# Kernel tuning notes

Hardware: AMD Instinct MI355X
Metric: run time of the kernel (lower is better)

The kernel has to match this reference:

```python
import jax, jax.numpy as jnp
import numpy as np

NEG_SLOPE = 0.2
BN_EPS = 1e-5


def setup_inputs() -> dict:
    key = jax.random.key(0)
    ks = jax.random.split(key, 10)
    N, E, F_IN, F_HID, F_OUT = 100000, 1600000, 64, 64, 32
    x = jax.random.normal(ks[0], (N, F_IN), dtype=jnp.float32)
    edge_index = jax.random.randint(ks[1], (2, E), 0, N, dtype=jnp.int64)
    s = 1.0 / np.sqrt(F_IN)
    W = jax.random.uniform(ks[2], (F_HID, F_IN), jnp.float32, -s, s)      # GATConv lin weight
    att_src = jax.random.uniform(ks[3], (F_HID,), jnp.float32, -s, s)
    att_dst = jax.random.uniform(ks[4], (F_HID,), jnp.float32, -s, s)
    conv_b = jnp.zeros((F_HID,), jnp.float32)
    gamma = jnp.ones((F_HID,), jnp.float32)
    beta = jnp.zeros((F_HID,), jnp.float32)
    s2 = 1.0 / np.sqrt(F_HID)
    fc_W = jax.random.uniform(ks[5], (F_OUT, F_HID), jnp.float32, -s2, s2)
    fc_b = jax.random.uniform(ks[6], (F_OUT,), jnp.float32, -s2, s2)
    return {"x": x, "edge_index": edge_index, "W": W, "att_src": att_src,
            "att_dst": att_dst, "conv_b": conv_b, "gamma": gamma, "beta": beta,
            "fc_W": fc_W, "fc_b": fc_b}


def _gat_conv(x, edge_index, W, att_src, att_dst, conv_b):
    N = x.shape[0]
    h = x @ W.T                                   # [N, C]
    a_src = h @ att_src                           # [N]
    a_dst = h @ att_dst                           # [N]
    loops = jnp.arange(N, dtype=edge_index.dtype)
    src = jnp.concatenate([edge_index[0], loops])  # add self-loops (PyG default)
    dst = jnp.concatenate([edge_index[1], loops])
    logits = jax.nn.leaky_relu(a_src[src] + a_dst[dst], NEG_SLOPE)  # [E+N]
    # segment softmax over incoming edges of each dst node
    seg_max = jax.ops.segment_max(logits, dst, num_segments=N)
    e = jnp.exp(logits - seg_max[dst])
    seg_sum = jax.ops.segment_sum(e, dst, num_segments=N)
    alpha = e / seg_sum[dst]                      # [E+N]
    msg = h[src] * alpha[:, None]                 # [E+N, C]
    out = jax.ops.segment_sum(msg, dst, num_segments=N)
    return out + conv_b


def reference(x, edge_index, W, att_src, att_dst, conv_b, gamma, beta, fc_W, fc_b):
    h = _gat_conv(x, edge_index, W, att_src, att_dst, conv_b)   # [N, hid]
    # BatchNorm1d (training-style batch statistics, biased variance)
    mu = jnp.mean(h, axis=0)
    var = jnp.var(h, axis=0)
    h = (h - mu) * jax.lax.rsqrt(var + BN_EPS) * gamma + beta
    h = jax.nn.relu(h)
    # dropout is identity in eval / deterministic reference
    return h @ fc_W.T + fc_b
```

## Files before the change

### kernel.cpp

```cpp
#include <hip/hip_runtime.h>
#include <hip/hip_bf16.h>

#define NEG_SLOPE 0.2f
#define BN_EPS 1e-5f
#define SCAN_CHUNK 4096
#define BSHIFT 8

__device__ __forceinline__ float lrelu(float x) { return x > 0.f ? x : NEG_SLOPE * x; }

__global__ void __launch_bounds__(256, 4) k_gemm_h(
    const float* __restrict__ x, const float* __restrict__ W,
    const float* __restrict__ att_src, const float* __restrict__ att_dst,
    const int* __restrict__ ei, float* __restrict__ h,
    float* __restrict__ aS, float* __restrict__ aD,
    int* __restrict__ deg, float* __restrict__ bnzero, int N, int E)
{
    __shared__ float4 xs[64][17];
    const int t = threadIdx.x;
    const int c = t & 63;
    const int wv = t >> 6;
    const int n0 = blockIdx.x * 64;

    float Wreg[64];
    const float4* Wp = (const float4*)W;
    #pragma unroll
    for (int k4 = 0; k4 < 16; ++k4) {
        float4 w4 = Wp[c * 16 + k4];
        Wreg[4*k4+0] = w4.x; Wreg[4*k4+1] = w4.y;
        Wreg[4*k4+2] = w4.z; Wreg[4*k4+3] = w4.w;
    }
    const float4* xp = (const float4*)x;
    #pragma unroll
    for (int i = 0; i < 4; ++i) {
        int idx = i * 256 + t;
        int row = idx >> 4, k4 = idx & 15;
        xs[row][k4] = (n0 + row < N) ? xp[(size_t)n0 * 16 + idx] : make_float4(0,0,0,0);
    }
    __syncthreads();

    const float asc = att_src[c], adc = att_dst[c];
    for (int i = 0; i < 16; ++i) {
        int nl = wv * 16 + i;
        int n = n0 + nl;
        if (n >= N) break;
        float a = 0.f;
        #pragma unroll
        for (int k4 = 0; k4 < 16; ++k4) {
            float4 xv = xs[nl][k4];
            a = fmaf(xv.x, Wreg[4*k4+0], a);
            a = fmaf(xv.y, Wreg[4*k4+1], a);
            a = fmaf(xv.z, Wreg[4*k4+2], a);
            a = fmaf(xv.w, Wreg[4*k4+3], a);
        }
        h[(size_t)n * 64 + c] = a;
        float s = a * asc, d = a * adc;
        #pragma unroll
        for (int off = 32; off; off >>= 1) { s += __shfl_xor(s, off); d += __shfl_xor(d, off); }
        if (c == 0) { aS[n] = s; aD[n] = d; }
    }
    int per = (E + gridDim.x - 1) / gridDim.x;
    int e0 = blockIdx.x * per;
    int e1 = min(e0 + per, E);
    for (int e = e0 + t; e < e1; e += 256) atomicAdd(&deg[ei[E + e]], 1);
    if (blockIdx.x == 0 && t < 128) bnzero[t] = 0.f;
}

__global__ void k_scan1(const int* __restrict__ deg, int* __restrict__ out,
                        int* __restrict__ bsum, int N)
{
    __shared__ int sh[256];
    const int t = threadIdx.x;
    const int base = blockIdx.x * SCAN_CHUNK + t * 16;
    int v[16];
    int run = 0;
    #pragma unroll
    for (int i = 0; i < 16; ++i) {
        int idx = base + i;
        v[i] = run;
        run += (idx < N) ? deg[idx] : 0;
    }
    sh[t] = run;
    __syncthreads();
    for (int off = 1; off < 256; off <<= 1) {
        int y = (t >= off) ? sh[t - off] : 0;
        __syncthreads();
        sh[t] += y;
        __syncthreads();
    }
    int texcl = (t == 0) ? 0 : sh[t - 1];
    #pragma unroll
    for (int i = 0; i < 16; ++i) {
        int idx = base + i;
        if (idx < N) out[idx] = texcl + v[i];
    }
    if (t == 255) bsum[blockIdx.x] = sh[255];
}

__global__ void k_scan2(int* __restrict__ bsum, const int* __restrict__ cursor,
                        int* __restrict__ bcur, int nb, int NB)
{
    __shared__ int sh[256];
    const int t = threadIdx.x;
    int v = (t < nb) ? bsum[t] : 0;
    sh[t] = v;
    __syncthreads();
    for (int off = 1; off < 256; off <<= 1) {
        int y = (t >= off) ? sh[t - off] : 0;
        __syncthreads();
        sh[t] += y;
        __syncthreads();
    }
    if (t < nb) bsum[t] = sh[t] - v;
    __syncthreads();
    for (int b = t; b < NB; b += 256) {
        int node = b << BSHIFT;
        bcur[b] = cursor[node] + bsum[node >> 12];
    }
}

__global__ void __launch_bounds__(256, 4) k_part1(
    const int* __restrict__ ei, int* __restrict__ bcur,
    unsigned* __restrict__ pairs, int E, int NB)
{
    __shared__ int hist[512], bbase[512], bofs[512];
    const int t = threadIdx.x;
    const int e0 = blockIdx.x * 4096;
    for (int i = t; i < NB; i += 256) hist[i] = 0;
    __syncthreads();
    int sv[16], dv[16];
    #pragma unroll
    for (int i = 0; i < 16; ++i) {
        int e = e0 + i * 256 + t;
        if (e < E) {
            sv[i] = ei[e];
            dv[i] = ei[E + e];
            atomicAdd(&hist[dv[i] >> BSHIFT], 1);
        } else dv[i] = -1;
    }
    __syncthreads();
    for (int i = t; i < NB; i += 256) {
        int hcnt = hist[i];
        bbase[i] = hcnt ? atomicAdd(&bcur[i], hcnt) : 0;
        bofs[i] = 0;
    }
    __syncthreads();
    #pragma unroll
    for (int i = 0; i < 16; ++i) {
        if (dv[i] >= 0) {
            int k = dv[i] >> BSHIFT;
            int o = atomicAdd(&bofs[k], 1);
            pairs[bbase[k] + o] = ((unsigned)sv[i] << BSHIFT) | (unsigned)(dv[i] & 255);
        }
    }
}

__global__ void __launch_bounds__(256, 4) k_part2(
    const unsigned* __restrict__ pairs, const int* __restrict__ cursor,
    const int* __restrict__ bsum, int* __restrict__ csr_src, int N, int E)
{
    __shared__ int cur[257];
    const int t = threadIdx.x;
    const int node0 = blockIdx.x << BSHIFT;
    for (int i = t; i <= 256; i += 256) {
        int node = node0 + i;
        cur[i] = (node < N) ? cursor[node] + bsum[node >> 12] : E;
    }
    __syncthreads();
    const int start = cur[0], end = cur[256];
    __syncthreads();
    for (int i = start + t; i < end; i += 256) {
        unsigned p = pairs[i];
        int pos = atomicAdd(&cur[p & 255], 1);
        csr_src[pos] = (int)(p >> BSHIFT);
    }
}

__global__ void __launch_bounds__(256, 8) k_aggregate(
    const int* __restrict__ csr_src, const int* __restrict__ cursor,
    const int* __restrict__ bsum, const int* __restrict__ deg,
    const float* __restrict__ aS, const float* __restrict__ aD,
    const float* __restrict__ h, const float* __restrict__ conv_b,
    float* __restrict__ hgat, float* __restrict__ bnsum, float* __restrict__ bnsq, int N)
{
    __shared__ float4 ps[256], pq[256];
    const int t = threadIdx.x;
    const int g = t & 15;
    const int grp = t >> 4;
    const int lb = (t & 63) & ~15;
    const float4* hp = (const float4*)h;
    const float4 bc = ((const float4*)conv_b)[g];
    float4 psum = make_float4(0,0,0,0), psq = make_float4(0,0,0,0);
    const int stride = gridDim.x * 16;

    for (int n = blockIdx.x * 16 + grp; n < N; n += stride) {
        const int dg = deg[n];
        const int start = cursor[n] + bsum[n >> 12];
        const int end = start + dg;
        const float aDn = aD[n];
        const float wself = __expf(lrelu(aS[n] + aDn));
        float4 hs = hp[(size_t)n * 16 + g];
        float4 acc;
        acc.x = wself * hs.x; acc.y = wself * hs.y;
        acc.z = wself * hs.z; acc.w = wself * hs.w;
        float wpart = (g == 0) ? wself : 0.f;

        for (int base = start; base < end; base += 16) {
            int cnt = end - base; cnt = cnt > 16 ? 16 : cnt;
            int   s_l = 0;
            float w_l = 0.f;
            if (g < cnt) {
                s_l = csr_src[base + g];
                w_l = __expf(lrelu(aS[s_l] + aDn));
                wpart += w_l;
                s_l <<= 4;
            }
            int j = 0;
            for (; j + 4 <= cnt; j += 4) {
                float w0 = __shfl(w_l, lb+j+0); int s0 = __shfl(s_l, lb+j+0);
                float w1 = __shfl(w_l, lb+j+1); int s1 = __shfl(s_l, lb+j+1);
                float w2 = __shfl(w_l, lb+j+2); int s2 = __shfl(s_l, lb+j+2);
                float w3 = __shfl(w_l, lb+j+3); int s3 = __shfl(s_l, lb+j+3);
                float4 h0 = hp[s0 + g];
                float4 h1 = hp[s1 + g];
                float4 h2 = hp[s2 + g];
                float4 h3 = hp[s3 + g];
                acc.x = fmaf(w0,h0.x,acc.x); acc.y = fmaf(w0,h0.y,acc.y);
                acc.z = fmaf(w0,h0.z,acc.z); acc.w = fmaf(w0,h0.w,acc.w);
                acc.x = fmaf(w1,h1.x,acc.x); acc.y = fmaf(w1,h1.y,acc.y);
                acc.z = fmaf(w1,h1.z,acc.z); acc.w = fmaf(w1,h1.w,acc.w);
                acc.x = fmaf(w2,h2.x,acc.x); acc.y = fmaf(w2,h2.y,acc.y);
                acc.z = fmaf(w2,h2.z,acc.z); acc.w = fmaf(w2,h2.w,acc.w);
                acc.x = fmaf(w3,h3.x,acc.x); acc.y = fmaf(w3,h3.y,acc.y);
                acc.z = fmaf(w3,h3.z,acc.z); acc.w = fmaf(w3,h3.w,acc.w);
            }
            for (; j < cnt; ++j) {
                float w0 = __shfl(w_l, lb+j); int s0 = __shfl(s_l, lb+j);
                float4 h0 = hp[s0 + g];
                acc.x = fmaf(w0,h0.x,acc.x); acc.y = fmaf(w0,h0.y,acc.y);
                acc.z = fmaf(w0,h0.z,acc.z); acc.w = fmaf(w0,h0.w,acc.w);
            }
        }
        #pragma unroll
        for (int off = 8; off; off >>= 1) wpart += __shfl_xor(wpart, off);
        float inv = 1.f / wpart;
        float4 v;
        v.x = fmaf(acc.x, inv, bc.x); v.y = fmaf(acc.y, inv, bc.y);
        v.z = fmaf(acc.z, inv, bc.z); v.w = fmaf(acc.w, inv, bc.w);
        ((float4*)hgat)[(size_t)n * 16 + g] = v;
        psum.x += v.x; psum.y += v.y; psum.z += v.z; psum.w += v.w;
        psq.x = fmaf(v.x,v.x,psq.x); psq.y = fmaf(v.y,v.y,psq.y);
        psq.z = fmaf(v.z,v.z,psq.z); psq.w = fmaf(v.w,v.w,psq.w);
    }
    ps[t] = psum; pq[t] = psq;
    __syncthreads();
    if (t < 64) {
        int gg = t >> 2, comp = t & 3;
        float s = 0.f, q = 0.f;
        #pragma unroll
        for (int k = 0; k < 16; ++k) {
            const float* pp = (const float*)&ps[k * 16 + gg];
            const float* qq = (const float*)&pq[k * 16 + gg];
            s += pp[comp]; q += qq[comp];
        }
        unsafeAtomicAdd(&bnsum[t], s);
        unsafeAtomicAdd(&bnsq[t], q);
    }
}

__global__ void k_bn_fc(const float* __restrict__ hg, const float* __restrict__ bnsum,
                        const float* __restrict__ bnsq, const float* __restrict__ gamma,
                        const float* __restrict__ beta, const float* __restrict__ fcW,
                        const float* __restrict__ fcb, float* __restrict__ out, int N)
{
    __shared__ float Ws[2048];
    __shared__ float sc[64], sh[64];
    const int t = threadIdx.x;
    for (int i = t; i < 2048; i += 256) Ws[i] = fcW[i];
    if (t < 64) {
        float invN = 1.f / (float)N;
        float mu  = bnsum[t] * invN;
        float var = bnsq[t] * invN - mu * mu;
        float s   = gamma[t] * rsqrtf(var + BN_EPS);
        sc[t] = s;
        sh[t] = beta[t] - mu * s;
    }
    __syncthreads();
    int n = blockIdx.x * 256 + t;
    if (n >= N) return;
    float y[64];
    const float4* hp = (const float4*)(hg + (size_t)n * 64);
    #pragma unroll
    for (int i = 0; i < 16; ++i) {
        float4 v = hp[i];
        y[4*i+0] = fmaxf(fmaf(v.x, sc[4*i+0], sh[4*i+0]), 0.f);
        y[4*i+1] = fmaxf(fmaf(v.y, sc[4*i+1], sh[4*i+1]), 0.f);
        y[4*i+2] = fmaxf(fmaf(v.z, sc[4*i+2], sh[4*i+2]), 0.f);
        y[4*i+3] = fmaxf(fmaf(v.w, sc[4*i+3], sh[4*i+3]), 0.f);
    }
    float4* op = (float4*)(out + (size_t)n * 32);
    #pragma unroll
    for (int o4 = 0; o4 < 8; ++o4) {
        float a0 = fcb[4*o4+0], a1 = fcb[4*o4+1], a2 = fcb[4*o4+2], a3 = fcb[4*o4+3];
        #pragma unroll
        for (int k = 0; k < 64; ++k) {
            float yv = y[k];
            a0 = fmaf(yv, Ws[(4*o4+0)*64+k], a0);
            a1 = fmaf(yv, Ws[(4*o4+1)*64+k], a1);
            a2 = fmaf(yv, Ws[(4*o4+2)*64+k], a2);
            a3 = fmaf(yv, Ws[(4*o4+3)*64+k], a3);
        }
        op[o4] = make_float4(a0, a1, a2, a3);
    }
}

extern "C" void kernel_launch(void* const* d_in, const int* in_sizes, int n_in,
                              void* d_out, int out_size, void* d_ws, size_t ws_size,
                              hipStream_t stream)
{
    const float* x       = (const float*)d_in[0];
    const int*   ei      = (const int*)d_in[1];
    const float* W       = (const float*)d_in[2];
    const float* att_src = (const float*)d_in[3];
    const float* att_dst = (const float*)d_in[4];
    const float* conv_b  = (const float*)d_in[5];
    const float* gamma   = (const float*)d_in[6];
    const float* beta    = (const float*)d_in[7];
    const float* fcW     = (const float*)d_in[8];
    const float* fcb     = (const float*)d_in[9];

    const int N = in_sizes[0] / 64;
    const int E = in_sizes[1] / 2;
    const int NB = (N + 255) >> BSHIFT;

    float* ws = (float*)d_ws;
    size_t N64 = (size_t)N * 64;
    float*    h       = ws;
    float*    hgat    = h + N64;
    float*    aS      = hgat + N64;
    float*    aD      = aS + N;
    float*    bnsum   = aD + N;
    float*    bnsq    = bnsum + 64;
    int*      deg     = (int*)(bnsq + 64);
    int*      cursor  = deg + N;
    int*      bsum    = cursor + N;
    int*      bcur    = bsum + 256;
    int*      csr_src = bcur + 512;
    unsigned* pairs   = (unsigned*)(csr_src + E);

    hipMemsetAsync(deg, 0, (size_t)N * sizeof(int), stream);

    k_gemm_h<<<(N + 63) / 64, 256, 0, stream>>>(x, W, att_src, att_dst, ei,
                                                h, aS, aD, deg, bnsum, N, E);
    int nb = (N + SCAN_CHUNK - 1) / SCAN_CHUNK;
    k_scan1<<<nb, 256, 0, stream>>>(deg, cursor, bsum, N);
    k_scan2<<<1, 256, 0, stream>>>(bsum, cursor, bcur, nb, NB);
    k_part1<<<(E + 4095) / 4096, 256, 0, stream>>>(ei, bcur, pairs, E, NB);
    k_part2<<<NB, 256, 0, stream>>>(pairs, cursor, bsum, csr_src, N, E);

    k_aggregate<<<2048, 256, 0, stream>>>(csr_src, cursor, bsum, deg, aS, aD, h,
                                          conv_b, hgat, bnsum, bnsq, N);
    k_bn_fc<<<(N + 255) / 256, 256, 0, stream>>>(hgat, bnsum, bnsq, gamma, beta,
                                                 fcW, fcb, (float*)d_out, N);
}
```

Baseline: 392.2 us.

## Store projected node features in bf16 and gather 8 channels per lane

The projected features h are now written as bf16 instead of fp32, which halves the bytes fetched by the random per-edge gathers in the aggregation kernel. The aggregation kernel is restructured so that 8 lanes each hold 8 channels and each wavefront covers 8 nodes instead of 4. Edges are consumed in batches of 8, and the BN partial-sum layout and launch bounds are adjusted to match. Rounding h to bf16 adds precision loss in the message sums, and each lane now keeps more accumulator registers.

```diff
diff --git a/kernel.cpp b/kernel.cpp
--- a/kernel.cpp
+++ b/kernel.cpp
@@ -7,11 +7,13 @@
 #define BSHIFT 8
 
 __device__ __forceinline__ float lrelu(float x) { return x > 0.f ? x : NEG_SLOPE * x; }
+__device__ __forceinline__ float bflo(unsigned u) { return __uint_as_float(u << 16); }
+__device__ __forceinline__ float bfhi(unsigned u) { return __uint_as_float(u & 0xffff0000u); }
 
 __global__ void __launch_bounds__(256, 4) k_gemm_h(
     const float* __restrict__ x, const float* __restrict__ W,
     const float* __restrict__ att_src, const float* __restrict__ att_dst,
-    const int* __restrict__ ei, float* __restrict__ h,
+    const int* __restrict__ ei, __hip_bfloat16* __restrict__ hb,
     float* __restrict__ aS, float* __restrict__ aD,
     int* __restrict__ deg, float* __restrict__ bnzero, int N, int E)
 {
@@ -52,7 +54,7 @@
             a = fmaf(xv.z, Wreg[4*k4+2], a);
             a = fmaf(xv.w, Wreg[4*k4+3], a);
         }
-        h[(size_t)n * 64 + c] = a;
+        hb[(size_t)n * 64 + c] = __float2bfloat16(a);
         float s = a * asc, d = a * adc;
         #pragma unroll
         for (int off = 32; off; off >>= 1) { s += __shfl_xor(s, off); d += __shfl_xor(d, off); }
@@ -175,44 +177,54 @@
     }
 }
 
-__global__ void __launch_bounds__(256, 8) k_aggregate(
+__global__ void __launch_bounds__(256, 6) k_aggregate(
     const int* __restrict__ csr_src, const int* __restrict__ cursor,
     const int* __restrict__ bsum, const int* __restrict__ deg,
     const float* __restrict__ aS, const float* __restrict__ aD,
-    const float* __restrict__ h, const float* __restrict__ conv_b,
+    const __hip_bfloat16* __restrict__ hb, const float* __restrict__ conv_b,
     float* __restrict__ hgat, float* __restrict__ bnsum, float* __restrict__ bnsq, int N)
 {
-    __shared__ float4 ps[256], pq[256];
-    const int t = threadIdx.x;
-    const int g = t & 15;
-    const int grp = t >> 4;
-    const int lb = (t & 63) & ~15;
-    const float4* hp = (const float4*)h;
-    const float4 bc = ((const float4*)conv_b)[g];
-    float4 psum = make_float4(0,0,0,0), psq = make_float4(0,0,0,0);
-    const int stride = gridDim.x * 16;
-
-    for (int n = blockIdx.x * 16 + grp; n < N; n += stride) {
+    __shared__ float ps[256][8], pq[256][8];
+    const int t = threadIdx.x;
+    const int g = t & 7;
+    const int grp = t >> 3;
+    const int lb = (t & 63) & ~7;
+    const uint4* hp = (const uint4*)hb;
+    float bc[8];
+    {
+        float4 b0 = ((const float4*)conv_b)[2*g+0];
+        float4 b1 = ((const float4*)conv_b)[2*g+1];
+        bc[0]=b0.x; bc[1]=b0.y; bc[2]=b0.z; bc[3]=b0.w;
+        bc[4]=b1.x; bc[5]=b1.y; bc[6]=b1.z; bc[7]=b1.w;
+    }
+    float psum[8], psq[8];
+    #pragma unroll
+    for (int j = 0; j < 8; ++j) { psum[j] = 0.f; psq[j] = 0.f; }
+    const int stride = gridDim.x * 32;
+
+    for (int n = blockIdx.x * 32 + grp; n < N; n += stride) {
         const int dg = deg[n];
         const int start = cursor[n] + bsum[n >> 12];
         const int end = start + dg;
         const float aDn = aD[n];
         const float wself = __expf(lrelu(aS[n] + aDn));
-        float4 hs = hp[(size_t)n * 16 + g];
-        float4 acc;
-        acc.x = wself * hs.x; acc.y = wself * hs.y;
-        acc.z = wself * hs.z; acc.w = wself * hs.w;
+        uint4 hs = hp[(size_t)n * 8 + g];
+        float acc[8];
+        acc[0] = wself * bflo(hs.x); acc[1] = wself * bfhi(hs.x);
+        acc[2] = wself * bflo(hs.y); acc[3] = wself * bfhi(hs.y);
+        acc[4] = wself * bflo(hs.z); acc[5] = wself * bfhi(hs.z);
+        acc[6] = wself * bflo(hs.w); acc[7] = wself * bfhi(hs.w);
         float wpart = (g == 0) ? wself : 0.f;
 
-        for (int base = start; base < end; base += 16) {
-            int cnt = end - base; cnt = cnt > 16 ? 16 : cnt;
+        for (int base = start; base < end; base += 8) {
+            int cnt = end - base; cnt = cnt > 8 ? 8 : cnt;
             int   s_l = 0;
             float w_l = 0.f;
             if (g < cnt) {
                 s_l = csr_src[base + g];
                 w_l = __expf(lrelu(aS[s_l] + aDn));
                 wpart += w_l;
-                s_l <<= 4;
+                s_l <<= 3;
             }
             int j = 0;
             for (; j + 4 <= cnt; j += 4) {
@@ -220,47 +232,61 @@
                 float w1 = __shfl(w_l, lb+j+1); int s1 = __shfl(s_l, lb+j+1);
                 float w2 = __shfl(w_l, lb+j+2); int s2 = __shfl(s_l, lb+j+2);
                 float w3 = __shfl(w_l, lb+j+3); int s3 = __shfl(s_l, lb+j+3);
-                float4 h0 = hp[s0 + g];
-                float4 h1 = hp[s1 + g];
-                float4 h2 = hp[s2 + g];
-                float4 h3 = hp[s3 + g];
-                acc.x = fmaf(w0,h0.x,acc.x); acc.y = fmaf(w0,h0.y,acc.y);
-                acc.z = fmaf(w0,h0.z,acc.z); acc.w = fmaf(w0,h0.w,acc.w);
-                acc.x = fmaf(w1,h1.x,acc.x); acc.y = fmaf(w1,h1.y,acc.y);
-                acc.z = fmaf(w1,h1.z,acc.z); acc.w = fmaf(w1,h1.w,acc.w);
-                acc.x = fmaf(w2,h2.x,acc.x); acc.y = fmaf(w2,h2.y,acc.y);
-                acc.z = fmaf(w2,h2.z,acc.z); acc.w = fmaf(w2,h2.w,acc.w);
-                acc.x = fmaf(w3,h3.x,acc.x); acc.y = fmaf(w3,h3.y,acc.y);
-                acc.z = fmaf(w3,h3.z,acc.z); acc.w = fmaf(w3,h3.w,acc.w);
+                uint4 q0 = hp[s0 + g];
+                uint4 q1 = hp[s1 + g];
+                uint4 q2 = hp[s2 + g];
+                uint4 q3 = hp[s3 + g];
+                acc[0]=fmaf(w0,bflo(q0.x),acc[0]); acc[1]=fmaf(w0,bfhi(q0.x),acc[1]);
+                acc[2]=fmaf(w0,bflo(q0.y),acc[2]); acc[3]=fmaf(w0,bfhi(q0.y),acc[3]);
+                acc[4]=fmaf(w0,bflo(q0.z),acc[4]); acc[5]=fmaf(w0,bfhi(q0.z),acc[5]);
+                acc[6]=fmaf(w0,bflo(q0.w),acc[6]); acc[7]=fmaf(w0,bfhi(q0.w),acc[7]);
+                acc[0]=fmaf(w1,bflo(q1.x),acc[0]); acc[1]=fmaf(w1,bfhi(q1.x),acc[1]);
+                acc[2]=fmaf(w1,bflo(q1.y),acc[2]); acc[3]=fmaf(w1,bfhi(q1.y),acc[3]);
+                acc[4]=fmaf(w1,bflo(q1.z),acc[4]); acc[5]=fmaf(w1,bfhi(q1.z),acc[5]);
+                acc[6]=fmaf(w1,bflo(q1.w),acc[6]); acc[7]=fmaf(w1,bfhi(q1.w),acc[7]);
+                acc[0]=fmaf(w2,bflo(q2.x),acc[0]); acc[1]=fmaf(w2,bfhi(q2.x),acc[1]);
+                acc[2]=fmaf(w2,bflo(q2.y),acc[2]); acc[3]=fmaf(w2,bfhi(q2.y),acc[3]);
+                acc[4]=fmaf(w2,bflo(q2.z),acc[4]); acc[5]=fmaf(w2,bfhi(q2.z),acc[5]);
+                acc[6]=fmaf(w2,bflo(q2.w),acc[6]); acc[7]=fmaf(w2,bfhi(q2.w),acc[7]);
+                acc[0]=fmaf(w3,bflo(q3.x),acc[0]); acc[1]=fmaf(w3,bfhi(q3.x),acc[1]);
+                acc[2]=fmaf(w3,bflo(q3.y),acc[2]); acc[3]=fmaf(w3,bfhi(q3.y),acc[3]);
+                acc[4]=fmaf(w3,bflo(q3.z),acc[4]); acc[5]=fmaf(w3,bfhi(q3.z),acc[5]);
+                acc[6]=fmaf(w3,bflo(q3.w),acc[6]); acc[7]=fmaf(w3,bfhi(q3.w),acc[7]);
             }
             for (; j < cnt; ++j) {
                 float w0 = __shfl(w_l, lb+j); int s0 = __shfl(s_l, lb+j);
-                float4 h0 = hp[s0 + g];
-                acc.x = fmaf(w0,h0.x,acc.x); acc.y = fmaf(w0,h0.y,acc.y);
-                acc.z = fmaf(w0,h0.z,acc.z); acc.w = fmaf(w0,h0.w,acc.w);
+                uint4 q0 = hp[s0 + g];
+                acc[0]=fmaf(w0,bflo(q0.x),acc[0]); acc[1]=fmaf(w0,bfhi(q0.x),acc[1]);
+                acc[2]=fmaf(w0,bflo(q0.y),acc[2]); acc[3]=fmaf(w0,bfhi(q0.y),acc[3]);
+                acc[4]=fmaf(w0,bflo(q0.z),acc[4]); acc[5]=fmaf(w0,bfhi(q0.z),acc[5]);
+                acc[6]=fmaf(w0,bflo(q0.w),acc[6]); acc[7]=fmaf(w0,bfhi(q0.w),acc[7]);
             }
         }
-        #pragma unroll
-        for (int off = 8; off; off >>= 1) wpart += __shfl_xor(wpart, off);
+        wpart += __shfl_xor(wpart, 1);
+        wpart += __shfl_xor(wpart, 2);
+        wpart += __shfl_xor(wpart, 4);
         float inv = 1.f / wpart;
-        float4 v;
-        v.x = fmaf(acc.x, inv, bc.x); v.y = fmaf(acc.y, inv, bc.y);
-        v.z = fmaf(acc.z, inv, bc.z); v.w = fmaf(acc.w, inv, bc.w);
-        ((float4*)hgat)[(size_t)n * 16 + g] = v;
-        psum.x += v.x; psum.y += v.y; psum.z += v.z; psum.w += v.w;
-        psq.x = fmaf(v.x,v.x,psq.x); psq.y = fmaf(v.y,v.y,psq.y);
-        psq.z = fmaf(v.z,v.z,psq.z); psq.w = fmaf(v.w,v.w,psq.w);
-    }
-    ps[t] = psum; pq[t] = psq;
+        float v[8];
+        #pragma unroll
+        for (int j = 0; j < 8; ++j) {
+            v[j] = fmaf(acc[j], inv, bc[j]);
+            psum[j] += v[j];
+            psq[j] = fmaf(v[j], v[j], psq[j]);
+        }
+        float4* op = (float4*)(hgat + (size_t)n * 64 + g * 8);
+        op[0] = make_float4(v[0], v[1], v[2], v[3]);
+        op[1] = make_float4(v[4], v[5], v[6], v[7]);
+    }
+    #pragma unroll
+    for (int j = 0; j < 8; ++j) { ps[t][j] = psum[j]; pq[t][j] = psq[j]; }
     __syncthreads();
     if (t < 64) {
-        int gg = t >> 2, comp = t & 3;
+        int p = t >> 3, j = t & 7;
         float s = 0.f, q = 0.f;
         #pragma unroll
-        for (int k = 0; k < 16; ++k) {
-            const float* pp = (const float*)&ps[k * 16 + gg];
-            const float* qq = (const float*)&pq[k * 16 + gg];
-            s += pp[comp]; q += qq[comp];
+        for (int k = 0; k < 32; ++k) {
+            s += ps[k * 8 + p][j];
+            q += pq[k * 8 + p][j];
         }
         unsafeAtomicAdd(&bnsum[t], s);
         unsafeAtomicAdd(&bnsq[t], q);
@@ -334,9 +360,9 @@
 
     float* ws = (float*)d_ws;
     size_t N64 = (size_t)N * 64;
-    float*    h       = ws;
-    float*    hgat    = h + N64;
-    float*    aS      = hgat + N64;
+    float*    hgat    = ws;
+    __hip_bfloat16* hb = (__hip_bfloat16*)(hgat + N64);
+    float*    aS      = hgat + N64 + N64 / 2;
     float*    aD      = aS + N;
     float*    bnsum   = aD + N;
     float*    bnsq    = bnsum + 64;
@@ -350,14 +376,14 @@
     hipMemsetAsync(deg, 0, (size_t)N * sizeof(int), stream);
 
     k_gemm_h<<<(N + 63) / 64, 256, 0, stream>>>(x, W, att_src, att_dst, ei,
-                                                h, aS, aD, deg, bnsum, N, E);
+                                                hb, aS, aD, deg, bnsum, N, E);
     int nb = (N + SCAN_CHUNK - 1) / SCAN_CHUNK;
     k_scan1<<<nb, 256, 0, stream>>>(deg, cursor, bsum, N);
     k_scan2<<<1, 256, 0, stream>>>(bsum, cursor, bcur, nb, NB);
     k_part1<<<(E + 4095) / 4096, 256, 0, stream>>>(ei, bcur, pairs, E, NB);
     k_part2<<<NB, 256, 0, stream>>>(pairs, cursor, bsum, csr_src, N, E);
 
-    k_aggregate<<<2048, 256, 0, stream>>>(csr_src, cursor, bsum, deg, aS, aD, h,
+    k_aggregate<<<2048, 256, 0, stream>>>(csr_src, cursor, bsum, deg, aS, aD, hb,
                                           conv_b, hgat, bnsum, bnsq, N);
     k_bn_fc<<<(N + 255) / 256, 256, 0, stream>>>(hgat, bnsum, bnsq, gamma, beta,
                                                  fcW, fcb, (float*)d_out, N);
```

Measured after the change: 367.6 us. 6.3% less time.
